# Kernel tuning notes

Hardware: AMD Instinct MI355X
Metric: run time of the kernel (lower is better)

The kernel has to match this reference:

```python
import jax, jax.numpy as jnp
import numpy as np

D_MODEL = 1024
NUM_HEADS = 16
D_HEAD = D_MODEL // NUM_HEADS


def setup_inputs() -> dict:
    key = jax.random.key(0)
    ks = jax.random.split(key, 9)
    s = 1.0 / np.sqrt(D_MODEL)
    return {
        "x": jax.random.normal(ks[0], (2, 2048, D_MODEL), dtype=jnp.float32),
        "Wq": jax.random.normal(ks[1], (D_MODEL, D_MODEL), dtype=jnp.float32) * s,
        "bq": jnp.zeros((D_MODEL,), dtype=jnp.float32),
        "Wk": jax.random.normal(ks[2], (D_MODEL, D_MODEL), dtype=jnp.float32) * s,
        "bk": jnp.zeros((D_MODEL,), dtype=jnp.float32),
        "Wv": jax.random.normal(ks[3], (D_MODEL, D_MODEL), dtype=jnp.float32) * s,
        "bv": jnp.zeros((D_MODEL,), dtype=jnp.float32),
        "Wo": jax.random.normal(ks[4], (D_MODEL, D_MODEL), dtype=jnp.float32) * s,
        "bo": jnp.zeros((D_MODEL,), dtype=jnp.float32),
    }


def reference(x, Wq, bq, Wk, bk, Wv, bv, Wo, bo):
    B, S, D = x.shape
    H, Dh = NUM_HEADS, D_HEAD

    def split_heads(t):  # [B,S,D] -> [B,H,S,Dh]
        return t.reshape(B, S, H, Dh).transpose(0, 2, 1, 3)

    # Linear layers: y = x @ W^T + b (torch nn.Linear convention)
    Q = split_heads(x @ Wq.T + bq)
    K = split_heads(x @ Wk.T + bk)
    V = split_heads(x @ Wv.T + bv)

    scale = 1.0 / jnp.sqrt(jnp.asarray(Dh, dtype=x.dtype))
    scores = jnp.einsum("bhqd,bhkd->bhqk", Q, K) * scale  # [B,H,S,S]
    attn = jax.nn.softmax(scores, axis=-1)
    context = jnp.einsum("bhqk,bhkd->bhqd", attn, V)  # [B,H,S,Dh]
    context = context.transpose(0, 2, 1, 3).reshape(B, S, D)
    return context @ Wo.T + bo
```

## Files before the change

### kernel.cpp

```cpp
#include <hip/hip_runtime.h>


#define T_TOK 4096
#define DM    1024
#define SQ    2048
#define NH    16
#define DH    64

typedef unsigned short u16;
typedef unsigned int   u32;
typedef __bf16 bf16x8 __attribute__((ext_vector_type(8)));
typedef float  f32x4  __attribute__((ext_vector_type(4)));
typedef float  f32x16 __attribute__((ext_vector_type(16)));
typedef u32    u32x4  __attribute__((ext_vector_type(4)));

__device__ __forceinline__ u16 f2bf(float f) {
  u32 u = __builtin_bit_cast(u32, f);
  u32 r = (u + 0x7FFFu + ((u >> 16) & 1u)) >> 16;
  return (u16)r;
}

#if __has_builtin(__builtin_amdgcn_cvt_pk_bf16_f32)
typedef __bf16 bf16x2 __attribute__((ext_vector_type(2)));
__device__ __forceinline__ u32 pk2bf(float a, float b) {
  bf16x2 h = __builtin_amdgcn_cvt_pk_bf16_f32(a, b);
  return __builtin_bit_cast(u32, h);
}
#else
__device__ __forceinline__ u32 pk2bf(float a, float b) {
  u32 r;
  asm("v_cvt_pk_bf16_f32 %0, %1, %2" : "=v"(r) : "v"(a), "v"(b));
  return r;
}
#endif

__device__ __forceinline__ void gld16(const void* g, void* l) {
  __builtin_amdgcn_global_load_lds(
      (const __attribute__((address_space(1))) u32*)g,
      (__attribute__((address_space(3))) u32*)l, 16, 0, 0);
}

__global__ void cast_bf16_kernel(const float* __restrict__ x,
    const float* __restrict__ w0, const float* __restrict__ w1,
    const float* __restrict__ w2, const float* __restrict__ w3,
    u16* __restrict__ xb, u16* __restrict__ o0, u16* __restrict__ o1,
    u16* __restrict__ o2, u16* __restrict__ o3)
{
  const float* src; u16* dst; int n;
  switch (blockIdx.y) {
    case 0:  src = x;  dst = xb; n = T_TOK * DM; break;
    case 1:  src = w0; dst = o0; n = DM * DM; break;
    case 2:  src = w1; dst = o1; n = DM * DM; break;
    case 3:  src = w2; dst = o2; n = DM * DM; break;
    default: src = w3; dst = o3; n = DM * DM; break;
  }
  const int stride = gridDim.x * blockDim.x;
  for (int i = blockIdx.x * blockDim.x + threadIdx.x; i * 4 < n; i += stride) {
    float4 v = ((const float4*)src)[i];
    ushort4 o;
    o.x = f2bf(v.x); o.y = f2bf(v.y); o.z = f2bf(v.z); o.w = f2bf(v.w);
    ((ushort4*)dst)[i] = o;
  }
}

__device__ __forceinline__ void gemm_core_128x128(
    u16* lds, const u16* __restrict__ Ab, const u16* __restrict__ Bb,
    f32x4 acc[4][4])
{
  u16* As = lds;
  u16* Bs = lds + 8192;
  const int tid = threadIdx.x, lane = tid & 63, w = tid >> 6;
  const int waveM = w >> 1, waveN = w & 1;
  const int col = lane & 15, quad = lane >> 4;
  const int srow = lane >> 3;
  const int sg0  = (lane & 7) ^ srow;

  for (int k0 = 0; k0 < DM; k0 += 64) {
    #pragma unroll
    for (int i = 0; i < 4; ++i) {
      const int rb = w * 32 + i * 8;
      const int sg = sg0 ^ ((rb >> 3) & 3);
      gld16(Ab + (size_t)(rb + srow) * DM + k0 + sg * 8, &As[rb * 64]);
      gld16(Bb + (size_t)(rb + srow) * DM + k0 + sg * 8, &Bs[rb * 64]);
    }
    __syncthreads();
    #pragma unroll
    for (int c = 0; c < 2; ++c) {
      bf16x8 af[4], bg[4];
      #pragma unroll
      for (int i = 0; i < 4; ++i) {
        const int row = waveM * 64 + i * 16 + col;
        const int gp = (c * 4 + quad) ^ (row & 7) ^ ((row >> 3) & 3);
        af[i] = *(const bf16x8*)&As[row * 64 + gp * 8];
      }
      #pragma unroll
      for (int j = 0; j < 4; ++j) {
        const int row = waveN * 64 + j * 16 + col;
        const int gp = (c * 4 + quad) ^ (row & 7) ^ ((row >> 3) & 3);
        bg[j] = *(const bf16x8*)&Bs[row * 64 + gp * 8];
      }
      #pragma unroll
      for (int i = 0; i < 4; ++i) {
        #pragma unroll
        for (int j = 0; j < 4; ++j)
          acc[i][j] = __builtin_amdgcn_mfma_f32_16x16x32_bf16(af[i], bg[j], acc[i][j], 0, 0, 0);
      }
    }
    __syncthreads();
  }
}

__device__ __forceinline__ void gemm_core_qk(
    u16* lds, const u16* __restrict__ Aq, const u16* __restrict__ Ak,
    const u16* __restrict__ Bb, f32x4 accQ[4][4], f32x4 accK[4][4])
{
  u16* As = lds;
  u16* A2 = lds + 8192;
  u16* Bs = lds + 16384;
  const int tid = threadIdx.x, lane = tid & 63, w = tid >> 6;
  const int waveM = w >> 1, waveN = w & 1;
  const int col = lane & 15, quad = lane >> 4;
  const int srow = lane >> 3;
  const int sg0  = (lane & 7) ^ srow;

  for (int k0 = 0; k0 < DM; k0 += 64) {
    #pragma unroll
    for (int i = 0; i < 4; ++i) {
      const int rb = w * 32 + i * 8;
      const int sg = sg0 ^ ((rb >> 3) & 3);
      const size_t off = (size_t)(rb + srow) * DM + k0 + sg * 8;
      gld16(Aq + off, &As[rb * 64]);
      gld16(Ak + off, &A2[rb * 64]);
      gld16(Bb + off, &Bs[rb * 64]);
    }
    __syncthreads();
    #pragma unroll
    for (int c = 0; c < 2; ++c) {
      bf16x8 af[4], ag[4], bg[4];
      #pragma unroll
      for (int i = 0; i < 4; ++i) {
        const int row = waveM * 64 + i * 16 + col;
        const int gp = (c * 4 + quad) ^ (row & 7) ^ ((row >> 3) & 3);
        af[i] = *(const bf16x8*)&As[row * 64 + gp * 8];
        ag[i] = *(const bf16x8*)&A2[row * 64 + gp * 8];
      }
      #pragma unroll
      for (int j = 0; j < 4; ++j) {
        const int row = waveN * 64 + j * 16 + col;
        const int gp = (c * 4 + quad) ^ (row & 7) ^ ((row >> 3) & 3);
        bg[j] = *(const bf16x8*)&Bs[row * 64 + gp * 8];
      }
      #pragma unroll
      for (int i = 0; i < 4; ++i) {
        #pragma unroll
        for (int j = 0; j < 4; ++j) {
          accQ[i][j] = __builtin_amdgcn_mfma_f32_16x16x32_bf16(af[i], bg[j], accQ[i][j], 0, 0, 0);
          accK[i][j] = __builtin_amdgcn_mfma_f32_16x16x32_bf16(ag[i], bg[j], accK[i][j], 0, 0, 0);
        }
      }
    }
    __syncthreads();
  }
}

__global__ __launch_bounds__(256, 2) void gemm_qkv_kernel(
    const u16* __restrict__ xb,
    const u16* __restrict__ Wqb, const u16* __restrict__ Wkb, const u16* __restrict__ Wvb,
    const float* __restrict__ bq, const float* __restrict__ bk, const float* __restrict__ bv,
    u16* __restrict__ Qs, u16* __restrict__ Kh, u16* __restrict__ Vt)
{
  __shared__ __align__(16) u16 smem[3 * 8192];
  const int z = blockIdx.z;
  const int tb = blockIdx.x;
  const int cb = blockIdx.y;

  const int tid = threadIdx.x;
  const int lane = tid & 63, w = tid >> 6;
  const int waveM = w >> 1, waveN = w & 1;
  const int col = lane & 15, quad = lane >> 4;
  const f32x4 zf = {0.f, 0.f, 0.f, 0.f};

  if (z == 1) {
    u16* tr = smem;
    f32x4 acc[4][4];
    #pragma unroll
    for (int i = 0; i < 4; ++i)
      #pragma unroll
      for (int j = 0; j < 4; ++j) acc[i][j] = zf;
    gemm_core_128x128(smem, xb + (size_t)(tb * 128) * DM,
                      Wvb + (size_t)(cb * 128) * DM, acc);
    #pragma unroll
    for (int j = 0; j < 4; ++j) {
      const int cl = waveN * 64 + j * 16 + col;
      const float bb = bv[cb * 128 + cl];
      #pragma unroll
      for (int i = 0; i < 4; ++i) {
        const int tl = waveM * 64 + i * 16 + quad * 4;
        ushort4 pk;
        pk.x = f2bf(acc[i][j][0] + bb); pk.y = f2bf(acc[i][j][1] + bb);
        pk.z = f2bf(acc[i][j][2] + bb); pk.w = f2bf(acc[i][j][3] + bb);
        *(ushort4*)&tr[cl * 136 + tl] = pk;
      }
    }
    __syncthreads();
    const int t0 = tb * 128;
    const int b = t0 >> 11, sBase = t0 & 2047;
    #pragma unroll
    for (int rep = 0; rep < 8; ++rep) {
      const int chunk = rep * 256 + tid;
      const int row = chunk >> 4, off = (chunk & 15) * 8;
      const int c = cb * 128 + row;
      const int h = c >> 6, d = c & 63;
      uint4 v = *(const uint4*)&tr[row * 136 + off];
      *(uint4*)&Vt[((size_t)(b * NH + h) * DH + d) * SQ + sBase + off] = v;
    }
  } else {
    f32x4 accQ[4][4], accK[4][4];
    #pragma unroll
    for (int i = 0; i < 4; ++i)
      #pragma unroll
      for (int j = 0; j < 4; ++j) { accQ[i][j] = zf; accK[i][j] = zf; }
    gemm_core_qk(smem, Wqb + (size_t)(cb * 128) * DM,
                 Wkb + (size_t)(cb * 128) * DM,
                 xb + (size_t)(tb * 128) * DM, accQ, accK);
    const float qscale = 0.18033688011112042f;
    const int chBase  = cb * 128 + waveM * 64;
    const int tokBase = tb * 128 + waveN * 64;
    #pragma unroll
    for (int i = 0; i < 4; ++i) {
      const int c0 = chBase + i * 16 + quad * 4;
      const int hh = c0 >> 6, d0 = c0 & 63;
      const float4 bbq = *(const float4*)&bq[c0];
      const float4 bbk = *(const float4*)&bk[c0];
      #pragma unroll
      for (int j = 0; j < 4; ++j) {
        const int t = tokBase + j * 16 + col;
        const int b = t >> 11, s = t & 2047;
        const size_t base = ((size_t)(b * NH + hh) * SQ + s) * DH + d0;
        ushort4 pq;
        pq.x = f2bf((accQ[i][j][0] + bbq.x) * qscale);
        pq.y = f2bf((accQ[i][j][1] + bbq.y) * qscale);
        pq.z = f2bf((accQ[i][j][2] + bbq.z) * qscale);
        pq.w = f2bf((accQ[i][j][3] + bbq.w) * qscale);
        *(ushort4*)&Qs[base] = pq;
        ushort4 pk;
        pk.x = f2bf(accK[i][j][0] + bbk.x);
        pk.y = f2bf(accK[i][j][1] + bbk.y);
        pk.z = f2bf(accK[i][j][2] + bbk.z);
        pk.w = f2bf(accK[i][j][3] + bbk.w);
        *(ushort4*)&Kh[base] = pk;
      }
    }
  }
}

__global__ __launch_bounds__(256, 2) void attn_kernel(
    const u16* __restrict__ Qs, const u16* __restrict__ Kh,
    const u16* __restrict__ Vt, u16* __restrict__ ctx)
{
  __shared__ __align__(16) char smem[32 * 1024];
  u16* KtB = (u16*)smem;
  u16* VlB = (u16*)(smem + 16384);

  const int tid = threadIdx.x, lane = tid & 63, w = tid >> 6;
  const int l31 = lane & 31, h = lane >> 5;
  const int bh = blockIdx.x, q0 = blockIdx.y * 128;
  const u16* Qb = Qs + ((size_t)bh * SQ + q0) * DH;
  const u16* Kb = Kh + (size_t)bh * SQ * DH;
  const u16* Vb = Vt + (size_t)bh * DH * SQ;
  const int srow = lane >> 3;
  const int sgl  = (lane & 7) ^ srow;

  bf16x8 qreg[4];
  #pragma unroll
  for (int ks = 0; ks < 4; ++ks)
    qreg[ks] = *(const bf16x8*)(Qb + (size_t)(w * 32 + l31) * DH + ks * 16 + h * 8);

  #pragma unroll
  for (int i = 0; i < 2; ++i) {
    const int rb = w * 16 + i * 8;
    const int sg = sgl ^ ((rb >> 3) & 3);
    gld16(Kb + (size_t)(rb + srow) * DH + sg * 8, &KtB[rb * 64]);
    gld16(Vb + (size_t)(rb + srow) * SQ + sg * 8, &VlB[rb * 64]);
  }

  f32x16 cacc[2];
  #pragma unroll
  for (int dt = 0; dt < 2; ++dt)
    #pragma unroll
    for (int e = 0; e < 16; ++e) cacc[dt][e] = 0.f;
  float l_s = 0.f;
  __syncthreads();

  for (int kt = 0; kt < SQ / 64; ++kt) {
    const int cur = kt & 1;
    u16* Kt = KtB + cur * 4096;
    u16* Vl = VlB + cur * 4096;
    if (kt + 1 < SQ / 64) {
      const int nxt = cur ^ 1, s1 = (kt + 1) * 64;
      u16* Ktn = KtB + nxt * 4096;
      u16* Vln = VlB + nxt * 4096;
      #pragma unroll
      for (int i = 0; i < 2; ++i) {
        const int rb = w * 16 + i * 8;
        const int sg = sgl ^ ((rb >> 3) & 3);
        gld16(Kb + (size_t)(s1 + rb + srow) * DH + sg * 8, &Ktn[rb * 64]);
        gld16(Vb + (size_t)(rb + srow) * SQ + s1 + sg * 8, &Vln[rb * 64]);
      }
    }

    f32x16 sacc0 = {}, sacc1 = {};
    __builtin_amdgcn_s_setprio(1);
    #pragma unroll
    for (int ks = 0; ks < 4; ++ks) {
      const int gp = ((2 * ks + h) ^ (l31 & 7) ^ ((l31 >> 3) & 3)) * 8;
      bf16x8 kf0 = *(const bf16x8*)&Kt[l31 * 64 + gp];
      bf16x8 kf1 = *(const bf16x8*)&Kt[(32 + l31) * 64 + gp];
      sacc0 = __builtin_amdgcn_mfma_f32_32x32x16_bf16(kf0, qreg[ks], sacc0, 0, 0, 0);
      sacc1 = __builtin_amdgcn_mfma_f32_32x32x16_bf16(kf1, qreg[ks], sacc1, 0, 0, 0);
    }
    __builtin_amdgcn_s_setprio(0);

    u32 Pp[2][4][2];
    {
      float p[16], q[16];
      #pragma unroll
      for (int e = 0; e < 16; ++e) {
        p[e] = __builtin_amdgcn_exp2f(sacc0[e]);
        q[e] = __builtin_amdgcn_exp2f(sacc1[e]);
      }
      float t0 = (p[0] + p[1]) + (p[2] + p[3]);
      float t1 = (p[4] + p[5]) + (p[6] + p[7]);
      float t2 = (p[8] + p[9]) + (p[10] + p[11]);
      float t3 = (p[12] + p[13]) + (p[14] + p[15]);
      float u0 = (q[0] + q[1]) + (q[2] + q[3]);
      float u1 = (q[4] + q[5]) + (q[6] + q[7]);
      float u2 = (q[8] + q[9]) + (q[10] + q[11]);
      float u3 = (q[12] + q[13]) + (q[14] + q[15]);
      l_s += ((t0 + t1) + (t2 + t3)) + ((u0 + u1) + (u2 + u3));
      #pragma unroll
      for (int rg = 0; rg < 4; ++rg) {
        Pp[0][rg][0] = pk2bf(p[4 * rg + 0], p[4 * rg + 1]);
        Pp[0][rg][1] = pk2bf(p[4 * rg + 2], p[4 * rg + 3]);
        Pp[1][rg][0] = pk2bf(q[4 * rg + 0], q[4 * rg + 1]);
        Pp[1][rg][1] = pk2bf(q[4 * rg + 2], q[4 * rg + 3]);
      }
    }

    __builtin_amdgcn_s_setprio(1);
    #pragma unroll
    for (int ksg = 0; ksg < 4; ++ksg) {
      const int hs = ksg >> 1, p2 = ksg & 1;
      u32 a0 = Pp[hs][2 * p2][0], b0 = Pp[hs][2 * p2 + 1][0];
      u32 a1 = Pp[hs][2 * p2][1], b1 = Pp[hs][2 * p2 + 1][1];
      asm("v_permlane32_swap_b32 %0, %1" : "+v"(a0), "+v"(b0));
      asm("v_permlane32_swap_b32 %0, %1" : "+v"(a1), "+v"(b1));
      u32x4 fw;
      fw.x = a0; fw.y = a1; fw.z = b0; fw.w = b1;
      bf16x8 pf = __builtin_bit_cast(bf16x8, fw);
      const int gp = ((2 * ksg + h) ^ (l31 & 7) ^ ((l31 >> 3) & 3)) * 8;
      bf16x8 vf0 = *(const bf16x8*)&Vl[l31 * 64 + gp];
      bf16x8 vf1 = *(const bf16x8*)&Vl[(32 + l31) * 64 + gp];
      cacc[0] = __builtin_amdgcn_mfma_f32_32x32x16_bf16(vf0, pf, cacc[0], 0, 0, 0);
      cacc[1] = __builtin_amdgcn_mfma_f32_32x32x16_bf16(vf1, pf, cacc[1], 0, 0, 0);
    }
    __builtin_amdgcn_s_setprio(0);
    __syncthreads();
  }

  const float lq = l_s + __shfl_xor(l_s, 32, 64);
  const float inv = 1.0f / lq;
  const int b = bh >> 4, hd = bh & 15;
  const int s = q0 + w * 32 + l31;
  #pragma unroll
  for (int dt = 0; dt < 2; ++dt) {
    #pragma unroll
    for (int c = 0; c < 4; ++c) {
      const int d0 = dt * 32 + c * 8 + 4 * h;
      ushort4 pk;
      pk.x = f2bf(cacc[dt][4 * c + 0] * inv);
      pk.y = f2bf(cacc[dt][4 * c + 1] * inv);
      pk.z = f2bf(cacc[dt][4 * c + 2] * inv);
      pk.w = f2bf(cacc[dt][4 * c + 3] * inv);
      *(ushort4*)&ctx[(size_t)(b * SQ + s) * DM + hd * DH + d0] = pk;
    }
  }
}

__device__ __forceinline__ void gemm_core_128x64(
    u16* lds, const u16* __restrict__ Ab, const u16* __restrict__ Bb,
    f32x4 acc[4][2])
{
  u16* As = lds;
  u16* Bs = lds + 8192;
  const int tid = threadIdx.x, lane = tid & 63, w = tid >> 6;
  const int waveM = w >> 1, waveN = w & 1;
  const int col = lane & 15, quad = lane >> 4;
  const int srow = lane >> 3;
  const int sg0  = (lane & 7) ^ srow;

  for (int k0 = 0; k0 < DM; k0 += 64) {
    #pragma unroll
    for (int i = 0; i < 4; ++i) {
      const int rb = w * 32 + i * 8;
      const int sg = sg0 ^ ((rb >> 3) & 3);
      gld16(Ab + (size_t)(rb + srow) * DM + k0 + sg * 8, &As[rb * 64]);
    }
    #pragma unroll
    for (int i = 0; i < 2; ++i) {
      const int rb = w * 16 + i * 8;
      const int sg = sg0 ^ ((rb >> 3) & 3);
      gld16(Bb + (size_t)(rb + srow) * DM + k0 + sg * 8, &Bs[rb * 64]);
    }
    __syncthreads();
    #pragma unroll
    for (int c = 0; c < 2; ++c) {
      bf16x8 af[4], bg[2];
      #pragma unroll
      for (int i = 0; i < 4; ++i) {
        const int row = waveM * 64 + i * 16 + col;
        const int gp = (c * 4 + quad) ^ (row & 7) ^ ((row >> 3) & 3);
        af[i] = *(const bf16x8*)&As[row * 64 + gp * 8];
      }
      #pragma unroll
      for (int j = 0; j < 2; ++j) {
        const int row = waveN * 32 + j * 16 + col;
        const int gp = (c * 4 + quad) ^ (row & 7) ^ ((row >> 3) & 3);
        bg[j] = *(const bf16x8*)&Bs[row * 64 + gp * 8];
      }
      #pragma unroll
      for (int i = 0; i < 4; ++i) {
        #pragma unroll
        for (int j = 0; j < 2; ++j)
          acc[i][j] = __builtin_amdgcn_mfma_f32_16x16x32_bf16(af[i], bg[j], acc[i][j], 0, 0, 0);
      }
    }
    __syncthreads();
  }
}

__global__ __launch_bounds__(256) void gemm_out_kernel(
    const u16* __restrict__ ctx, const u16* __restrict__ Wob,
    const float* __restrict__ bo, float* __restrict__ out)
{
  __shared__ __align__(16) u16 smem[128 * 64 + 64 * 64];
  const int tb = blockIdx.x;
  const int cb = blockIdx.y;
  const int tid = threadIdx.x, lane = tid & 63, w = tid >> 6;
  const int waveM = w >> 1, waveN = w & 1;
  const int col = lane & 15, quad = lane >> 4;

  f32x4 acc[4][2];
  const f32x4 zf = {0.f, 0.f, 0.f, 0.f};
  #pragma unroll
  for (int i = 0; i < 4; ++i) {
    #pragma unroll
    for (int j = 0; j < 2; ++j) acc[i][j] = zf;
  }

  gemm_core_128x64(smem, ctx + (size_t)(tb * 128) * DM,
                   Wob + (size_t)(cb * 64) * DM, acc);

  const int rowBase = tb * 128 + waveM * 64;
  const int colBase = cb * 64 + waveN * 32;
  #pragma unroll
  for (int j = 0; j < 2; ++j) {
    const int c = colBase + j * 16 + col;
    const float bb = bo[c];
    #pragma unroll
    for (int i = 0; i < 4; ++i) {
      #pragma unroll
      for (int r = 0; r < 4; ++r) {
        const int t = rowBase + i * 16 + quad * 4 + r;
        out[(size_t)t * DM + c] = acc[i][j][r] + bb;
      }
    }
  }
}

extern "C" void kernel_launch(void* const* d_in, const int* in_sizes, int n_in,
                              void* d_out, int out_size, void* d_ws, size_t ws_size,
                              hipStream_t stream) {
  const float* x  = (const float*)d_in[0];
  const float* Wq = (const float*)d_in[1];
  const float* bq = (const float*)d_in[2];
  const float* Wk = (const float*)d_in[3];
  const float* bk = (const float*)d_in[4];
  const float* Wv = (const float*)d_in[5];
  const float* bv = (const float*)d_in[6];
  const float* Wo = (const float*)d_in[7];
  const float* bo = (const float*)d_in[8];

  char* ws = (char*)d_ws;
  u16* xb  = (u16*)(ws);
  u16* Wqb = (u16*)(ws + (8ull  << 20));
  u16* Wkb = (u16*)(ws + (10ull << 20));
  u16* Wvb = (u16*)(ws + (12ull << 20));
  u16* Wob = (u16*)(ws + (14ull << 20));
  u16* Qs  = (u16*)(ws + (16ull << 20));
  u16* Kh  = (u16*)(ws + (24ull << 20));
  u16* Vt  = (u16*)(ws + (32ull << 20));
  u16* ctx = xb;

  cast_bf16_kernel<<<dim3(256, 5), 256, 0, stream>>>(x, Wq, Wk, Wv, Wo,
                                                     xb, Wqb, Wkb, Wvb, Wob);
  gemm_qkv_kernel<<<dim3(32, 8, 2), 256, 0, stream>>>(xb, Wqb, Wkb, Wvb,
                                                      bq, bk, bv, Qs, Kh, Vt);
  attn_kernel<<<dim3(32, 16), 256, 0, stream>>>(Qs, Kh, Vt, ctx);
  gemm_out_kernel<<<dim3(32, 16), 256, 0, stream>>>(ctx, Wob, bo, (float*)d_out);
  (void)in_sizes; (void)n_in; (void)out_size; (void)ws_size;
}
```

Measured before the change: 180.7 us.

## Fuse Q/K/V projections into one 512-thread block with double-buffered LDS

Replaces the two-way split (QK blocks and separate V blocks) with a single 512-thread block that computes Q, K and V for a 128x128 tile, so the x tile is loaded once and shared across all three weight tiles. The k-loop now double-buffers LDS, prefetching the next K-slice via async global-to-LDS loads while MFMAs run on the current one. This cuts redundant x traffic and hides load latency. In exchange the grid halves to 256 blocks, LDS use rises to 128KB per block, which limits occupancy, and V transposition now uses scalar LDS stores.

```diff
diff --git a/kernel.cpp b/kernel.cpp
--- a/kernel.cpp
+++ b/kernel.cpp
@@ -63,194 +63,141 @@
   }
 }
 
-__device__ __forceinline__ void gemm_core_128x128(
-    u16* lds, const u16* __restrict__ Ab, const u16* __restrict__ Bb,
-    f32x4 acc[4][4])
-{
-  u16* As = lds;
-  u16* Bs = lds + 8192;
-  const int tid = threadIdx.x, lane = tid & 63, w = tid >> 6;
-  const int waveM = w >> 1, waveN = w & 1;
-  const int col = lane & 15, quad = lane >> 4;
-  const int srow = lane >> 3;
-  const int sg0  = (lane & 7) ^ srow;
-
-  for (int k0 = 0; k0 < DM; k0 += 64) {
-    #pragma unroll
-    for (int i = 0; i < 4; ++i) {
-      const int rb = w * 32 + i * 8;
-      const int sg = sg0 ^ ((rb >> 3) & 3);
-      gld16(Ab + (size_t)(rb + srow) * DM + k0 + sg * 8, &As[rb * 64]);
-      gld16(Bb + (size_t)(rb + srow) * DM + k0 + sg * 8, &Bs[rb * 64]);
-    }
-    __syncthreads();
-    #pragma unroll
-    for (int c = 0; c < 2; ++c) {
-      bf16x8 af[4], bg[4];
-      #pragma unroll
-      for (int i = 0; i < 4; ++i) {
-        const int row = waveM * 64 + i * 16 + col;
-        const int gp = (c * 4 + quad) ^ (row & 7) ^ ((row >> 3) & 3);
-        af[i] = *(const bf16x8*)&As[row * 64 + gp * 8];
-      }
-      #pragma unroll
-      for (int j = 0; j < 4; ++j) {
-        const int row = waveN * 64 + j * 16 + col;
-        const int gp = (c * 4 + quad) ^ (row & 7) ^ ((row >> 3) & 3);
-        bg[j] = *(const bf16x8*)&Bs[row * 64 + gp * 8];
-      }
-      #pragma unroll
-      for (int i = 0; i < 4; ++i) {
-        #pragma unroll
-        for (int j = 0; j < 4; ++j)
-          acc[i][j] = __builtin_amdgcn_mfma_f32_16x16x32_bf16(af[i], bg[j], acc[i][j], 0, 0, 0);
-      }
-    }
-    __syncthreads();
-  }
-}
-
-__device__ __forceinline__ void gemm_core_qk(
-    u16* lds, const u16* __restrict__ Aq, const u16* __restrict__ Ak,
-    const u16* __restrict__ Bb, f32x4 accQ[4][4], f32x4 accK[4][4])
-{
-  u16* As = lds;
-  u16* A2 = lds + 8192;
-  u16* Bs = lds + 16384;
-  const int tid = threadIdx.x, lane = tid & 63, w = tid >> 6;
-  const int waveM = w >> 1, waveN = w & 1;
-  const int col = lane & 15, quad = lane >> 4;
-  const int srow = lane >> 3;
-  const int sg0  = (lane & 7) ^ srow;
-
-  for (int k0 = 0; k0 < DM; k0 += 64) {
-    #pragma unroll
-    for (int i = 0; i < 4; ++i) {
-      const int rb = w * 32 + i * 8;
-      const int sg = sg0 ^ ((rb >> 3) & 3);
-      const size_t off = (size_t)(rb + srow) * DM + k0 + sg * 8;
-      gld16(Aq + off, &As[rb * 64]);
-      gld16(Ak + off, &A2[rb * 64]);
-      gld16(Bb + off, &Bs[rb * 64]);
-    }
-    __syncthreads();
-    #pragma unroll
-    for (int c = 0; c < 2; ++c) {
-      bf16x8 af[4], ag[4], bg[4];
-      #pragma unroll
-      for (int i = 0; i < 4; ++i) {
-        const int row = waveM * 64 + i * 16 + col;
-        const int gp = (c * 4 + quad) ^ (row & 7) ^ ((row >> 3) & 3);
-        af[i] = *(const bf16x8*)&As[row * 64 + gp * 8];
-        ag[i] = *(const bf16x8*)&A2[row * 64 + gp * 8];
-      }
-      #pragma unroll
-      for (int j = 0; j < 4; ++j) {
-        const int row = waveN * 64 + j * 16 + col;
-        const int gp = (c * 4 + quad) ^ (row & 7) ^ ((row >> 3) & 3);
-        bg[j] = *(const bf16x8*)&Bs[row * 64 + gp * 8];
-      }
-      #pragma unroll
-      for (int i = 0; i < 4; ++i) {
-        #pragma unroll
-        for (int j = 0; j < 4; ++j) {
-          accQ[i][j] = __builtin_amdgcn_mfma_f32_16x16x32_bf16(af[i], bg[j], accQ[i][j], 0, 0, 0);
-          accK[i][j] = __builtin_amdgcn_mfma_f32_16x16x32_bf16(ag[i], bg[j], accK[i][j], 0, 0, 0);
-        }
-      }
-    }
-    __syncthreads();
-  }
-}
-
-__global__ __launch_bounds__(256, 2) void gemm_qkv_kernel(
+__global__ __launch_bounds__(512, 2) void gemm_qkv_kernel(
     const u16* __restrict__ xb,
     const u16* __restrict__ Wqb, const u16* __restrict__ Wkb, const u16* __restrict__ Wvb,
     const float* __restrict__ bq, const float* __restrict__ bk, const float* __restrict__ bv,
     u16* __restrict__ Qs, u16* __restrict__ Kh, u16* __restrict__ Vt)
 {
-  __shared__ __align__(16) u16 smem[3 * 8192];
-  const int z = blockIdx.z;
+  __shared__ __align__(16) u16 smem[2][4][8192];
   const int tb = blockIdx.x;
   const int cb = blockIdx.y;
-
   const int tid = threadIdx.x;
   const int lane = tid & 63, w = tid >> 6;
-  const int waveM = w >> 1, waveN = w & 1;
+  const int waveM = w >> 2, waveN = w & 3;
   const int col = lane & 15, quad = lane >> 4;
+  const int srow = lane >> 3;
+  const int sg0  = (lane & 7) ^ srow;
+
+  const u16* psrc;
+  switch (w >> 1) {
+    case 0:  psrc = Wqb + (size_t)(cb * 128) * DM; break;
+    case 1:  psrc = Wkb + (size_t)(cb * 128) * DM; break;
+    case 2:  psrc = Wvb + (size_t)(cb * 128) * DM; break;
+    default: psrc = xb  + (size_t)(tb * 128) * DM; break;
+  }
+  const int sp = w >> 1;
+  const int sh = (w & 1) * 64;
+
+  #define QKV_STAGE(buf_, k0_) do {                                          \
+    _Pragma("unroll")                                                        \
+    for (int i_ = 0; i_ < 8; ++i_) {                                         \
+      const int rb_ = sh + i_ * 8;                                           \
+      const int sg_ = sg0 ^ ((rb_ >> 3) & 3);                                \
+      gld16(psrc + (size_t)(rb_ + srow) * DM + (k0_) + sg_ * 8,              \
+            &smem[buf_][sp][rb_ * 64]);                                      \
+    }                                                                        \
+  } while (0)
+
+  f32x4 accQ[4][2], accK[4][2], accV[4][2];
   const f32x4 zf = {0.f, 0.f, 0.f, 0.f};
-
-  if (z == 1) {
-    u16* tr = smem;
-    f32x4 acc[4][4];
-    #pragma unroll
-    for (int i = 0; i < 4; ++i)
-      #pragma unroll
-      for (int j = 0; j < 4; ++j) acc[i][j] = zf;
-    gemm_core_128x128(smem, xb + (size_t)(tb * 128) * DM,
-                      Wvb + (size_t)(cb * 128) * DM, acc);
-    #pragma unroll
-    for (int j = 0; j < 4; ++j) {
-      const int cl = waveN * 64 + j * 16 + col;
-      const float bb = bv[cb * 128 + cl];
+  #pragma unroll
+  for (int i = 0; i < 4; ++i) {
+    #pragma unroll
+    for (int j = 0; j < 2; ++j) { accQ[i][j] = zf; accK[i][j] = zf; accV[i][j] = zf; }
+  }
+
+  QKV_STAGE(0, 0);
+  __syncthreads();
+  int buf = 0;
+  for (int k0 = 0; k0 < DM; k0 += 64) {
+    if (k0 + 64 < DM) QKV_STAGE(buf ^ 1, k0 + 64);
+    #pragma unroll
+    for (int c = 0; c < 2; ++c) {
+      bf16x8 aq[4], ak[4], av[4], bg[2];
       #pragma unroll
       for (int i = 0; i < 4; ++i) {
-        const int tl = waveM * 64 + i * 16 + quad * 4;
-        ushort4 pk;
-        pk.x = f2bf(acc[i][j][0] + bb); pk.y = f2bf(acc[i][j][1] + bb);
-        pk.z = f2bf(acc[i][j][2] + bb); pk.w = f2bf(acc[i][j][3] + bb);
-        *(ushort4*)&tr[cl * 136 + tl] = pk;
+        const int row = waveM * 64 + i * 16 + col;
+        const int gp = ((c * 4 + quad) ^ (row & 7) ^ ((row >> 3) & 3)) * 8;
+        aq[i] = *(const bf16x8*)&smem[buf][0][row * 64 + gp];
+        ak[i] = *(const bf16x8*)&smem[buf][1][row * 64 + gp];
+        av[i] = *(const bf16x8*)&smem[buf][2][row * 64 + gp];
+      }
+      #pragma unroll
+      for (int j = 0; j < 2; ++j) {
+        const int row = waveN * 32 + j * 16 + col;
+        const int gp = ((c * 4 + quad) ^ (row & 7) ^ ((row >> 3) & 3)) * 8;
+        bg[j] = *(const bf16x8*)&smem[buf][3][row * 64 + gp];
+      }
+      #pragma unroll
+      for (int i = 0; i < 4; ++i) {
+        #pragma unroll
+        for (int j = 0; j < 2; ++j) {
+          accQ[i][j] = __builtin_amdgcn_mfma_f32_16x16x32_bf16(aq[i], bg[j], accQ[i][j], 0, 0, 0);
+          accK[i][j] = __builtin_amdgcn_mfma_f32_16x16x32_bf16(ak[i], bg[j], accK[i][j], 0, 0, 0);
+          accV[i][j] = __builtin_amdgcn_mfma_f32_16x16x32_bf16(av[i], bg[j], accV[i][j], 0, 0, 0);
+        }
       }
     }
     __syncthreads();
-    const int t0 = tb * 128;
-    const int b = t0 >> 11, sBase = t0 & 2047;
-    #pragma unroll
-    for (int rep = 0; rep < 8; ++rep) {
-      const int chunk = rep * 256 + tid;
-      const int row = chunk >> 4, off = (chunk & 15) * 8;
-      const int c = cb * 128 + row;
-      const int h = c >> 6, d = c & 63;
-      uint4 v = *(const uint4*)&tr[row * 136 + off];
-      *(uint4*)&Vt[((size_t)(b * NH + h) * DH + d) * SQ + sBase + off] = v;
-    }
-  } else {
-    f32x4 accQ[4][4], accK[4][4];
-    #pragma unroll
-    for (int i = 0; i < 4; ++i)
-      #pragma unroll
-      for (int j = 0; j < 4; ++j) { accQ[i][j] = zf; accK[i][j] = zf; }
-    gemm_core_qk(smem, Wqb + (size_t)(cb * 128) * DM,
-                 Wkb + (size_t)(cb * 128) * DM,
-                 xb + (size_t)(tb * 128) * DM, accQ, accK);
-    const float qscale = 0.18033688011112042f;
-    const int chBase  = cb * 128 + waveM * 64;
-    const int tokBase = tb * 128 + waveN * 64;
-    #pragma unroll
-    for (int i = 0; i < 4; ++i) {
-      const int c0 = chBase + i * 16 + quad * 4;
-      const int hh = c0 >> 6, d0 = c0 & 63;
-      const float4 bbq = *(const float4*)&bq[c0];
-      const float4 bbk = *(const float4*)&bk[c0];
-      #pragma unroll
-      for (int j = 0; j < 4; ++j) {
-        const int t = tokBase + j * 16 + col;
-        const int b = t >> 11, s = t & 2047;
-        const size_t base = ((size_t)(b * NH + hh) * SQ + s) * DH + d0;
-        ushort4 pq;
-        pq.x = f2bf((accQ[i][j][0] + bbq.x) * qscale);
-        pq.y = f2bf((accQ[i][j][1] + bbq.y) * qscale);
-        pq.z = f2bf((accQ[i][j][2] + bbq.z) * qscale);
-        pq.w = f2bf((accQ[i][j][3] + bbq.w) * qscale);
-        *(ushort4*)&Qs[base] = pq;
-        ushort4 pk;
-        pk.x = f2bf(accK[i][j][0] + bbk.x);
-        pk.y = f2bf(accK[i][j][1] + bbk.y);
-        pk.z = f2bf(accK[i][j][2] + bbk.z);
-        pk.w = f2bf(accK[i][j][3] + bbk.w);
-        *(ushort4*)&Kh[base] = pk;
-      }
-    }
+    buf ^= 1;
+  }
+  #undef QKV_STAGE
+
+  const float qscale = 0.18033688011112042f;
+  const int chBase  = cb * 128 + waveM * 64;
+  const int tokBase = tb * 128 + waveN * 32;
+  #pragma unroll
+  for (int i = 0; i < 4; ++i) {
+    const int c0 = chBase + i * 16 + quad * 4;
+    const int hh = c0 >> 6, d0 = c0 & 63;
+    const float4 bbq = *(const float4*)&bq[c0];
+    const float4 bbk = *(const float4*)&bk[c0];
+    #pragma unroll
+    for (int j = 0; j < 2; ++j) {
+      const int t = tokBase + j * 16 + col;
+      const int b = t >> 11, s = t & 2047;
+      const size_t base = ((size_t)(b * NH + hh) * SQ + s) * DH + d0;
+      ushort4 pq;
+      pq.x = f2bf((accQ[i][j][0] + bbq.x) * qscale);
+      pq.y = f2bf((accQ[i][j][1] + bbq.y) * qscale);
+      pq.z = f2bf((accQ[i][j][2] + bbq.z) * qscale);
+      pq.w = f2bf((accQ[i][j][3] + bbq.w) * qscale);
+      *(ushort4*)&Qs[base] = pq;
+      ushort4 pk;
+      pk.x = f2bf(accK[i][j][0] + bbk.x);
+      pk.y = f2bf(accK[i][j][1] + bbk.y);
+      pk.z = f2bf(accK[i][j][2] + bbk.z);
+      pk.w = f2bf(accK[i][j][3] + bbk.w);
+      *(ushort4*)&Kh[base] = pk;
+    }
+  }
+
+  u16* tr = (u16*)smem;
+  #pragma unroll
+  for (int i = 0; i < 4; ++i) {
+    const int c0 = waveM * 64 + i * 16 + quad * 4;
+    const float4 bbv = *(const float4*)&bv[cb * 128 + c0];
+    #pragma unroll
+    for (int j = 0; j < 2; ++j) {
+      const int tok = waveN * 32 + j * 16 + col;
+      tr[(c0 + 0) * 136 + tok] = f2bf(accV[i][j][0] + bbv.x);
+      tr[(c0 + 1) * 136 + tok] = f2bf(accV[i][j][1] + bbv.y);
+      tr[(c0 + 2) * 136 + tok] = f2bf(accV[i][j][2] + bbv.z);
+      tr[(c0 + 3) * 136 + tok] = f2bf(accV[i][j][3] + bbv.w);
+    }
+  }
+  __syncthreads();
+  const int t0 = tb * 128;
+  const int b = t0 >> 11, sBase = t0 & 2047;
+  #pragma unroll
+  for (int rep = 0; rep < 4; ++rep) {
+    const int chunk = rep * 512 + tid;
+    const int row = chunk >> 4, off = (chunk & 15) * 8;
+    const int c = cb * 128 + row;
+    const int hh = c >> 6, d = c & 63;
+    uint4 v = *(const uint4*)&tr[row * 136 + off];
+    *(uint4*)&Vt[((size_t)(b * NH + hh) * DH + d) * SQ + sBase + off] = v;
   }
 }
 
@@ -504,8 +451,8 @@
 
   cast_bf16_kernel<<<dim3(256, 5), 256, 0, stream>>>(x, Wq, Wk, Wv, Wo,
                                                      xb, Wqb, Wkb, Wvb, Wob);
-  gemm_qkv_kernel<<<dim3(32, 8, 2), 256, 0, stream>>>(xb, Wqb, Wkb, Wvb,
-                                                      bq, bk, bv, Qs, Kh, Vt);
+  gemm_qkv_kernel<<<dim3(32, 8), 512, 0, stream>>>(xb, Wqb, Wkb, Wvb,
+                                                   bq, bk, bv, Qs, Kh, Vt);
   attn_kernel<<<dim3(32, 16), 256, 0, stream>>>(Qs, Kh, Vt, ctx);
   gemm_out_kernel<<<dim3(32, 16), 256, 0, stream>>>(ctx, Wob, bo, (float*)d_out);
   (void)in_sizes; (void)n_in; (void)out_size; (void)ws_size;
```

Result: no change. 183.3 us (+1.4%).

## Fuse V projection into dual-tile QK core and widen attention blocks to eight waves

Applied to the files above, without the earlier changes.

The QKV GEMM now runs on a single 48x8 grid. The V blocks reuse the dual-accumulator QK core so one Wv tile serves two 128-token x tiles, which balances work with the Q/K blocks and removes the separate 128x128 core. The attention kernel moves to 512-thread blocks covering 256 queries, with each wave loading one 8-row slice of K/V, so every K/V tile staged in LDS is shared by twice as many query rows. The trade-off is fewer attention blocks (256), higher register pressure under launch_bounds(512,2), and a larger per-block V epilogue.

```diff
diff --git a/kernel.cpp b/kernel.cpp
--- a/kernel.cpp
+++ b/kernel.cpp
@@ -60,53 +60,6 @@
     ushort4 o;
     o.x = f2bf(v.x); o.y = f2bf(v.y); o.z = f2bf(v.z); o.w = f2bf(v.w);
     ((ushort4*)dst)[i] = o;
-  }
-}
-
-__device__ __forceinline__ void gemm_core_128x128(
-    u16* lds, const u16* __restrict__ Ab, const u16* __restrict__ Bb,
-    f32x4 acc[4][4])
-{
-  u16* As = lds;
-  u16* Bs = lds + 8192;
-  const int tid = threadIdx.x, lane = tid & 63, w = tid >> 6;
-  const int waveM = w >> 1, waveN = w & 1;
-  const int col = lane & 15, quad = lane >> 4;
-  const int srow = lane >> 3;
-  const int sg0  = (lane & 7) ^ srow;
-
-  for (int k0 = 0; k0 < DM; k0 += 64) {
-    #pragma unroll
-    for (int i = 0; i < 4; ++i) {
-      const int rb = w * 32 + i * 8;
-      const int sg = sg0 ^ ((rb >> 3) & 3);
-      gld16(Ab + (size_t)(rb + srow) * DM + k0 + sg * 8, &As[rb * 64]);
-      gld16(Bb + (size_t)(rb + srow) * DM + k0 + sg * 8, &Bs[rb * 64]);
-    }
-    __syncthreads();
-    #pragma unroll
-    for (int c = 0; c < 2; ++c) {
-      bf16x8 af[4], bg[4];
-      #pragma unroll
-      for (int i = 0; i < 4; ++i) {
-        const int row = waveM * 64 + i * 16 + col;
-        const int gp = (c * 4 + quad) ^ (row & 7) ^ ((row >> 3) & 3);
-        af[i] = *(const bf16x8*)&As[row * 64 + gp * 8];
-      }
-      #pragma unroll
-      for (int j = 0; j < 4; ++j) {
-        const int row = waveN * 64 + j * 16 + col;
-        const int gp = (c * 4 + quad) ^ (row & 7) ^ ((row >> 3) & 3);
-        bg[j] = *(const bf16x8*)&Bs[row * 64 + gp * 8];
-      }
-      #pragma unroll
-      for (int i = 0; i < 4; ++i) {
-        #pragma unroll
-        for (int j = 0; j < 4; ++j)
-          acc[i][j] = __builtin_amdgcn_mfma_f32_16x16x32_bf16(af[i], bg[j], acc[i][j], 0, 0, 0);
-      }
-    }
-    __syncthreads();
   }
 }
 
@@ -170,59 +123,24 @@
     u16* __restrict__ Qs, u16* __restrict__ Kh, u16* __restrict__ Vt)
 {
   __shared__ __align__(16) u16 smem[3 * 8192];
-  const int z = blockIdx.z;
-  const int tb = blockIdx.x;
   const int cb = blockIdx.y;
-
   const int tid = threadIdx.x;
   const int lane = tid & 63, w = tid >> 6;
   const int waveM = w >> 1, waveN = w & 1;
   const int col = lane & 15, quad = lane >> 4;
   const f32x4 zf = {0.f, 0.f, 0.f, 0.f};
 
-  if (z == 1) {
-    u16* tr = smem;
-    f32x4 acc[4][4];
-    #pragma unroll
-    for (int i = 0; i < 4; ++i)
-      #pragma unroll
-      for (int j = 0; j < 4; ++j) acc[i][j] = zf;
-    gemm_core_128x128(smem, xb + (size_t)(tb * 128) * DM,
-                      Wvb + (size_t)(cb * 128) * DM, acc);
-    #pragma unroll
-    for (int j = 0; j < 4; ++j) {
-      const int cl = waveN * 64 + j * 16 + col;
-      const float bb = bv[cb * 128 + cl];
-      #pragma unroll
-      for (int i = 0; i < 4; ++i) {
-        const int tl = waveM * 64 + i * 16 + quad * 4;
-        ushort4 pk;
-        pk.x = f2bf(acc[i][j][0] + bb); pk.y = f2bf(acc[i][j][1] + bb);
-        pk.z = f2bf(acc[i][j][2] + bb); pk.w = f2bf(acc[i][j][3] + bb);
-        *(ushort4*)&tr[cl * 136 + tl] = pk;
-      }
-    }
-    __syncthreads();
-    const int t0 = tb * 128;
-    const int b = t0 >> 11, sBase = t0 & 2047;
-    #pragma unroll
-    for (int rep = 0; rep < 8; ++rep) {
-      const int chunk = rep * 256 + tid;
-      const int row = chunk >> 4, off = (chunk & 15) * 8;
-      const int c = cb * 128 + row;
-      const int h = c >> 6, d = c & 63;
-      uint4 v = *(const uint4*)&tr[row * 136 + off];
-      *(uint4*)&Vt[((size_t)(b * NH + h) * DH + d) * SQ + sBase + off] = v;
-    }
-  } else {
-    f32x4 accQ[4][4], accK[4][4];
-    #pragma unroll
-    for (int i = 0; i < 4; ++i)
-      #pragma unroll
-      for (int j = 0; j < 4; ++j) { accQ[i][j] = zf; accK[i][j] = zf; }
+  f32x4 accA[4][4], accB[4][4];
+  #pragma unroll
+  for (int i = 0; i < 4; ++i)
+    #pragma unroll
+    for (int j = 0; j < 4; ++j) { accA[i][j] = zf; accB[i][j] = zf; }
+
+  if (blockIdx.x < 32) {
+    const int tb = blockIdx.x;
     gemm_core_qk(smem, Wqb + (size_t)(cb * 128) * DM,
                  Wkb + (size_t)(cb * 128) * DM,
-                 xb + (size_t)(tb * 128) * DM, accQ, accK);
+                 xb + (size_t)(tb * 128) * DM, accA, accB);
     const float qscale = 0.18033688011112042f;
     const int chBase  = cb * 128 + waveM * 64;
     const int tokBase = tb * 128 + waveN * 64;
@@ -238,23 +156,59 @@
         const int b = t >> 11, s = t & 2047;
         const size_t base = ((size_t)(b * NH + hh) * SQ + s) * DH + d0;
         ushort4 pq;
-        pq.x = f2bf((accQ[i][j][0] + bbq.x) * qscale);
-        pq.y = f2bf((accQ[i][j][1] + bbq.y) * qscale);
-        pq.z = f2bf((accQ[i][j][2] + bbq.z) * qscale);
-        pq.w = f2bf((accQ[i][j][3] + bbq.w) * qscale);
+        pq.x = f2bf((accA[i][j][0] + bbq.x) * qscale);
+        pq.y = f2bf((accA[i][j][1] + bbq.y) * qscale);
+        pq.z = f2bf((accA[i][j][2] + bbq.z) * qscale);
+        pq.w = f2bf((accA[i][j][3] + bbq.w) * qscale);
         *(ushort4*)&Qs[base] = pq;
         ushort4 pk;
-        pk.x = f2bf(accK[i][j][0] + bbk.x);
-        pk.y = f2bf(accK[i][j][1] + bbk.y);
-        pk.z = f2bf(accK[i][j][2] + bbk.z);
-        pk.w = f2bf(accK[i][j][3] + bbk.w);
+        pk.x = f2bf(accB[i][j][0] + bbk.x);
+        pk.y = f2bf(accB[i][j][1] + bbk.y);
+        pk.z = f2bf(accB[i][j][2] + bbk.z);
+        pk.w = f2bf(accB[i][j][3] + bbk.w);
         *(ushort4*)&Kh[base] = pk;
       }
     }
-  }
-}
-
-__global__ __launch_bounds__(256, 2) void attn_kernel(
+  } else {
+    const int tp = blockIdx.x - 32;
+    gemm_core_qk(smem, xb + (size_t)(tp * 256) * DM,
+                 xb + (size_t)(tp * 256 + 128) * DM,
+                 Wvb + (size_t)(cb * 128) * DM, accA, accB);
+    u16* tr = smem;
+    #pragma unroll
+    for (int pass = 0; pass < 2; ++pass) {
+      f32x4 (*acc)[4] = pass ? accB : accA;
+      #pragma unroll
+      for (int j = 0; j < 4; ++j) {
+        const int cl = waveN * 64 + j * 16 + col;
+        const float bb = bv[cb * 128 + cl];
+        #pragma unroll
+        for (int i = 0; i < 4; ++i) {
+          const int tl = waveM * 64 + i * 16 + quad * 4;
+          ushort4 pk;
+          pk.x = f2bf(acc[i][j][0] + bb); pk.y = f2bf(acc[i][j][1] + bb);
+          pk.z = f2bf(acc[i][j][2] + bb); pk.w = f2bf(acc[i][j][3] + bb);
+          *(ushort4*)&tr[cl * 136 + tl] = pk;
+        }
+      }
+      __syncthreads();
+      const int t0 = tp * 256 + pass * 128;
+      const int b = t0 >> 11, sBase = t0 & 2047;
+      #pragma unroll
+      for (int rep = 0; rep < 8; ++rep) {
+        const int chunk = rep * 256 + tid;
+        const int row = chunk >> 4, off = (chunk & 15) * 8;
+        const int c = cb * 128 + row;
+        const int hh = c >> 6, d = c & 63;
+        uint4 v = *(const uint4*)&tr[row * 136 + off];
+        *(uint4*)&Vt[((size_t)(b * NH + hh) * DH + d) * SQ + sBase + off] = v;
+      }
+      __syncthreads();
+    }
+  }
+}
+
+__global__ __launch_bounds__(512, 2) void attn_kernel(
     const u16* __restrict__ Qs, const u16* __restrict__ Kh,
     const u16* __restrict__ Vt, u16* __restrict__ ctx)
 {
@@ -264,25 +218,22 @@
 
   const int tid = threadIdx.x, lane = tid & 63, w = tid >> 6;
   const int l31 = lane & 31, h = lane >> 5;
-  const int bh = blockIdx.x, q0 = blockIdx.y * 128;
+  const int bh = blockIdx.x, q0 = blockIdx.y * 256;
   const u16* Qb = Qs + ((size_t)bh * SQ + q0) * DH;
   const u16* Kb = Kh + (size_t)bh * SQ * DH;
   const u16* Vb = Vt + (size_t)bh * DH * SQ;
   const int srow = lane >> 3;
   const int sgl  = (lane & 7) ^ srow;
+  const int rb   = w * 8;
+  const int sg   = sgl ^ (w & 3);
 
   bf16x8 qreg[4];
   #pragma unroll
   for (int ks = 0; ks < 4; ++ks)
     qreg[ks] = *(const bf16x8*)(Qb + (size_t)(w * 32 + l31) * DH + ks * 16 + h * 8);
 
-  #pragma unroll
-  for (int i = 0; i < 2; ++i) {
-    const int rb = w * 16 + i * 8;
-    const int sg = sgl ^ ((rb >> 3) & 3);
-    gld16(Kb + (size_t)(rb + srow) * DH + sg * 8, &KtB[rb * 64]);
-    gld16(Vb + (size_t)(rb + srow) * SQ + sg * 8, &VlB[rb * 64]);
-  }
+  gld16(Kb + (size_t)(rb + srow) * DH + sg * 8, &KtB[rb * 64]);
+  gld16(Vb + (size_t)(rb + srow) * SQ + sg * 8, &VlB[rb * 64]);
 
   f32x16 cacc[2];
   #pragma unroll
@@ -298,15 +249,8 @@
     u16* Vl = VlB + cur * 4096;
     if (kt + 1 < SQ / 64) {
       const int nxt = cur ^ 1, s1 = (kt + 1) * 64;
-      u16* Ktn = KtB + nxt * 4096;
-      u16* Vln = VlB + nxt * 4096;
-      #pragma unroll
-      for (int i = 0; i < 2; ++i) {
-        const int rb = w * 16 + i * 8;
-        const int sg = sgl ^ ((rb >> 3) & 3);
-        gld16(Kb + (size_t)(s1 + rb + srow) * DH + sg * 8, &Ktn[rb * 64]);
-        gld16(Vb + (size_t)(rb + srow) * SQ + s1 + sg * 8, &Vln[rb * 64]);
-      }
+      gld16(Kb + (size_t)(s1 + rb + srow) * DH + sg * 8, &KtB[nxt * 4096 + rb * 64]);
+      gld16(Vb + (size_t)(rb + srow) * SQ + s1 + sg * 8, &VlB[nxt * 4096 + rb * 64]);
     }
 
     f32x16 sacc0 = {}, sacc1 = {};
@@ -504,9 +448,9 @@
 
   cast_bf16_kernel<<<dim3(256, 5), 256, 0, stream>>>(x, Wq, Wk, Wv, Wo,
                                                      xb, Wqb, Wkb, Wvb, Wob);
-  gemm_qkv_kernel<<<dim3(32, 8, 2), 256, 0, stream>>>(xb, Wqb, Wkb, Wvb,
-                                                      bq, bk, bv, Qs, Kh, Vt);
-  attn_kernel<<<dim3(32, 16), 256, 0, stream>>>(Qs, Kh, Vt, ctx);
+  gemm_qkv_kernel<<<dim3(48, 8), 256, 0, stream>>>(xb, Wqb, Wkb, Wvb,
+                                                   bq, bk, bv, Qs, Kh, Vt);
+  attn_kernel<<<dim3(32, 8), 512, 0, stream>>>(Qs, Kh, Vt, ctx);
   gemm_out_kernel<<<dim3(32, 16), 256, 0, stream>>>(ctx, Wob, bo, (float*)d_out);
   (void)in_sizes; (void)n_in; (void)out_size; (void)ws_size;
 }
```

Result: no change. 182.2 us (+0.9%).
